# Kernel optimization log

Measured on AMD Instinct MI355X. Metric: run time of the kernel, lower is better.

The kernel has to match this reference:

```python
import jax, jax.numpy as jnp
import numpy as np

D, DK, DV, H = 1024, 64, 1024, 16
DVH = DV // H  # per-head value dim
EPS = 1e-5


def _layer_norm(x, g, b):
    mu = jnp.mean(x, axis=-1, keepdims=True)
    var = jnp.var(x, axis=-1, keepdims=True)
    return (x - mu) * jax.lax.rsqrt(var + EPS) * g + b


def setup_inputs() -> dict:
    key = jax.random.key(0)
    ks = jax.random.split(key, 12)
    s = lambda k, shape, fan_in: jax.random.normal(k, shape, jnp.float32) / np.sqrt(fan_in)
    return {
        "x": jax.random.normal(ks[0], (2, 2048, D), jnp.float32),
        "Wq": s(ks[1], (H, D, DK), D),
        "Wk": s(ks[2], (H, D, DK), D),
        "Wv": s(ks[3], (H, D, DVH), D),
        "Wo": s(ks[4], (DV, D), DV),
        "ln1_g": jnp.ones((D,), jnp.float32),
        "ln1_b": jnp.zeros((D,), jnp.float32),
        "W1": s(ks[5], (D, 4 * D), D),
        "b1": jnp.zeros((4 * D,), jnp.float32),
        "W2": s(ks[6], (4 * D, D), 4 * D),
        "b2": jnp.zeros((D,), jnp.float32),
        "ln2_g": jnp.ones((D,), jnp.float32),
        "ln2_b": jnp.zeros((D,), jnp.float32),
    }


def reference(x, Wq, Wk, Wv, Wo, ln1_g, ln1_b, W1, b1, W2, b2, ln2_g, ln2_b):
    B, S, _ = x.shape
    # per-head projections (vectorized over the head loop of the original)
    q = jnp.einsum("bsd,hdk->bhsk", x, Wq)
    k = jnp.einsum("bsd,hdk->bhsk", x, Wk)
    v = jnp.einsum("bsd,hdv->bhsv", x, Wv)
    scores = jnp.einsum("bhsk,bhtk->bhst", q, k) / np.sqrt(DK).astype(np.float32)
    attn = jax.nn.softmax(scores, axis=-1)
    o = jnp.einsum("bhst,bhtv->bhsv", attn, v)  # [B,H,S,DVH]
    o = o.transpose(0, 2, 1, 3).reshape(B, S, DV)  # concat heads
    attn_out = o @ Wo
    x1 = _layer_norm(attn_out + x, ln1_g, ln1_b)
    ffn = jax.nn.relu(x1 @ W1 + b1) @ W2 + b2
    return _layer_norm(ffn + x1, ln2_g, ln2_b)
```

## Files before the change

### kernel.cpp

```cpp
#include <hip/hip_runtime.h>
#include <hip/hip_bf16.h>

typedef unsigned short u16;
typedef unsigned int u32;
typedef short short8 __attribute__((ext_vector_type(8)));
typedef float fx4 __attribute__((ext_vector_type(4)));
typedef u32 ux4 __attribute__((ext_vector_type(4)));

__device__ __forceinline__ float b2f(u16 x) {
  return __uint_as_float(((u32)x) << 16);
}
__device__ __forceinline__ u16 f2b(float f) {
  u32 u = __float_as_uint(f);
  u += 0x7fffu + ((u >> 16) & 1u);
  return (u16)(u >> 16);
}
__device__ __forceinline__ u32 cvtpk(float a, float b) {
  u32 r;
  asm("v_cvt_pk_bf16_f32 %0, %1, %2" : "=v"(r) : "v"(a), "v"(b));
  return r;
}

__device__ __forceinline__ void load16(const u16* g, u16* l) {
  __builtin_amdgcn_global_load_lds(
      (__attribute__((address_space(1))) void*)(u16*)g,
      (__attribute__((address_space(3))) void*)l, 16, 0, 0);
}

__global__ __launch_bounds__(256) void cvt_f2b_kernel(
    const float* __restrict__ in, u16* __restrict__ out)
{
  int i = (blockIdx.x * 256 + threadIdx.x) * 4;
  fx4 v = *(const fx4*)(in + i);
  u16 o4[4];
#pragma unroll
  for (int j = 0; j < 4; ++j) o4[j] = f2b(v[j]);
  *(uint2*)(out + i) = *(uint2*)o4;
}

__global__ __launch_bounds__(256) void transpose_f2b_kernel(
    const float* __restrict__ in, u16* __restrict__ out,
    int R, int C, int out_ld)
{
  __shared__ __align__(16) u16 tile[32][33];
  int tx = threadIdx.x, ty = threadIdx.y;
  int c0 = blockIdx.x * 32, r0 = blockIdx.y * 32;
  const float* inb = in + (size_t)blockIdx.z * R * C;
  u16* outb = out + (size_t)blockIdx.z * C * out_ld;
#pragma unroll
  for (int i = 0; i < 4; ++i)
    tile[ty + i * 8][tx] = f2b(inb[(size_t)(r0 + ty + i * 8) * C + c0 + tx]);
  __syncthreads();
#pragma unroll
  for (int i = 0; i < 4; ++i)
    outb[(size_t)(c0 + ty + i * 8) * out_ld + r0 + tx] = tile[tx][ty + i * 8];
}

__global__ __launch_bounds__(256) void transpose_b2b_kernel(
    const u16* __restrict__ in, u16* __restrict__ out, int in_ld, int out_ld)
{
  __shared__ __align__(16) u16 tile[32][33];
  int tx = threadIdx.x, ty = threadIdx.y;
  int c0 = blockIdx.x * 32, r0 = blockIdx.y * 32;
#pragma unroll
  for (int i = 0; i < 4; ++i)
    tile[ty + i * 8][tx] = in[(size_t)(r0 + ty + i * 8) * in_ld + c0 + tx];
  __syncthreads();
#pragma unroll
  for (int i = 0; i < 4; ++i)
    out[(size_t)(c0 + ty + i * 8) * out_ld + r0 + tx] = tile[tx][ty + i * 8];
}

__global__ __launch_bounds__(256, 2) void gemm_bt(
    const u16* __restrict__ A, const u16* __restrict__ BT,
    const float* __restrict__ bias, void* __restrict__ Cp,
    int M, int N, int K, int flags)
{
  __shared__ __align__(16) u16 As[2][4096];
  __shared__ __align__(16) u16 Bs[2][4096];
  int tid = threadIdx.x;
  int lane = tid & 63, wid = tid >> 6;
  int l15 = lane & 15, quad = lane >> 4;
  int wm = wid >> 1, wn = wid & 1;
  int m0 = blockIdx.y * 128, n0 = blockIdx.x * 128;

  int srow = wid * 16 + (lane >> 2);
  int sswz = (((lane >> 2) & 3) + ((lane >> 4) & 3)) & 3;
  int gch = (lane & 3) ^ sswz;
  const u16* gA = A + (size_t)(m0 + srow) * K + gch * 8;
  const u16* gB = BT + (size_t)(n0 + srow) * K + gch * 8;
  size_t gstep = (size_t)64 * K;
  u16* lA = &As[0][wid * 512];
  u16* lB = &Bs[0][wid * 512];

  int rswz = ((l15 & 3) + (l15 >> 2)) & 3;
  int rphys = ((quad ^ rswz) & 3) << 3;

  fx4 acc[4][4];
#pragma unroll
  for (int i = 0; i < 4; ++i)
#pragma unroll
    for (int j = 0; j < 4; ++j) acc[i][j] = fx4{0.f, 0.f, 0.f, 0.f};

  int nt = K >> 5;
  load16(gA,         lA);
  load16(gA + gstep, lA + 2048);
  load16(gB,         lB);
  load16(gB + gstep, lB + 2048);

  for (int kt = 0; kt < nt; ++kt) {
    __syncthreads();
    if (kt + 1 < nt) {
      int buf = (kt + 1) & 1;
      const u16* ga = gA + (kt + 1) * 32;
      const u16* gb = gB + (kt + 1) * 32;
      load16(ga,         lA + buf * 4096);
      load16(ga + gstep, lA + buf * 4096 + 2048);
      load16(gb,         lB + buf * 4096);
      load16(gb + gstep, lB + buf * 4096 + 2048);
    }
    const u16* Ab = As[kt & 1];
    const u16* Bb = Bs[kt & 1];
    short8 af[4], bf[4];
#pragma unroll
    for (int t = 0; t < 4; ++t)
      af[t] = *(const short8*)&Ab[(wm * 64 + t * 16 + l15) * 32 + rphys];
#pragma unroll
    for (int t = 0; t < 4; ++t)
      bf[t] = *(const short8*)&Bb[(wn * 64 + t * 16 + l15) * 32 + rphys];
#pragma unroll
    for (int tm = 0; tm < 4; ++tm)
#pragma unroll
      for (int tn = 0; tn < 4; ++tn)
        acc[tm][tn] = __builtin_amdgcn_mfma_f32_16x16x32_bf16(
            af[tm], bf[tn], acc[tm][tn], 0, 0, 0);
  }

  bool obf = flags & 1, hb = flags & 2, rl = flags & 4;
#pragma unroll
  for (int tn = 0; tn < 4; ++tn) {
    int col = n0 + wn * 64 + tn * 16 + l15;
    float bv = hb ? bias[col] : 0.0f;
#pragma unroll
    for (int tm = 0; tm < 4; ++tm) {
      int row = m0 + wm * 64 + tm * 16 + (quad << 2);
#pragma unroll
      for (int r = 0; r < 4; ++r) {
        float v = acc[tm][tn][r] + bv;
        if (rl) v = fmaxf(v, 0.0f);
        size_t idx = (size_t)(row + r) * N + col;
        if (obf) ((u16*)Cp)[idx] = f2b(v);
        else ((float*)Cp)[idx] = v;
      }
    }
  }
}

__global__ __launch_bounds__(256, 2) void gemm_bt_n64(
    const u16* __restrict__ A, const u16* __restrict__ BT,
    const float* __restrict__ bias, void* __restrict__ Cp,
    int M, int N, int K, int flags)
{
  __shared__ __align__(16) u16 As[2][4096];
  __shared__ __align__(16) u16 Bs[2][2048];
  int tid = threadIdx.x;
  int lane = tid & 63, wid = tid >> 6;
  int l15 = lane & 15, quad = lane >> 4;
  int wm = wid >> 1, wn = wid & 1;
  int m0 = blockIdx.y * 128, n0 = blockIdx.x * 64;
  int zz = blockIdx.z;
  int kc = K / (int)gridDim.z;

  int srow = wid * 16 + (lane >> 2);
  int sswz = (((lane >> 2) & 3) + ((lane >> 4) & 3)) & 3;
  int gch = (lane & 3) ^ sswz;
  const u16* gA = A + (size_t)(m0 + srow) * K + zz * kc + gch * 8;
  const u16* gB = BT + (size_t)(n0 + srow) * K + zz * kc + gch * 8;
  size_t gstep = (size_t)64 * K;
  u16* lA = &As[0][wid * 512];
  u16* lB = &Bs[0][wid * 512];

  int rswz = ((l15 & 3) + (l15 >> 2)) & 3;
  int rphys = ((quad ^ rswz) & 3) << 3;

  fx4 acc[4][2];
#pragma unroll
  for (int i = 0; i < 4; ++i)
#pragma unroll
    for (int j = 0; j < 2; ++j) acc[i][j] = fx4{0.f, 0.f, 0.f, 0.f};

  int nt = kc >> 5;
  load16(gA,         lA);
  load16(gA + gstep, lA + 2048);
  load16(gB,         lB);

  for (int kt = 0; kt < nt; ++kt) {
    __syncthreads();
    if (kt + 1 < nt) {
      int buf = (kt + 1) & 1;
      const u16* ga = gA + (kt + 1) * 32;
      const u16* gb = gB + (kt + 1) * 32;
      load16(ga,         lA + buf * 4096);
      load16(ga + gstep, lA + buf * 4096 + 2048);
      load16(gb,         lB + buf * 2048);
    }
    const u16* Ab = As[kt & 1];
    const u16* Bb = Bs[kt & 1];
    short8 af[4], bf[2];
#pragma unroll
    for (int t = 0; t < 4; ++t)
      af[t] = *(const short8*)&Ab[(wm * 64 + t * 16 + l15) * 32 + rphys];
#pragma unroll
    for (int t = 0; t < 2; ++t)
      bf[t] = *(const short8*)&Bb[(wn * 32 + t * 16 + l15) * 32 + rphys];
#pragma unroll
    for (int tm = 0; tm < 4; ++tm)
#pragma unroll
      for (int tn = 0; tn < 2; ++tn)
        acc[tm][tn] = __builtin_amdgcn_mfma_f32_16x16x32_bf16(
            af[tm], bf[tn], acc[tm][tn], 0, 0, 0);
  }

  bool obf = flags & 1, hb = flags & 2, rl = flags & 4;
  u16* cb16 = (u16*)Cp + (size_t)zz * M * N;
  float* cf32 = (float*)Cp + (size_t)zz * M * N;
#pragma unroll
  for (int tn = 0; tn < 2; ++tn) {
    int col = n0 + wn * 32 + tn * 16 + l15;
    float bv = hb ? bias[col] : 0.0f;
#pragma unroll
    for (int tm = 0; tm < 4; ++tm) {
      int row = m0 + wm * 64 + tm * 16 + (quad << 2);
#pragma unroll
      for (int r = 0; r < 4; ++r) {
        float v = acc[tm][tn][r] + bv;
        if (rl) v = fmaxf(v, 0.0f);
        size_t idx = (size_t)(row + r) * N + col;
        if (obf) cb16[idx] = f2b(v);
        else cf32[idx] = v;
      }
    }
  }
}

__global__ __launch_bounds__(256) void attn_kernel(
    const u16* __restrict__ qkv, const u16* __restrict__ vT,
    u16* __restrict__ o)
{
  __shared__ __align__(16) u16 Ks[2][4096];
  __shared__ __align__(16) u16 Vs[2][4096];
  int tid = threadIdx.x;
  int lane = tid & 63, wid = tid >> 6;
  int l15 = lane & 15, quad = lane >> 4;
  int b = blockIdx.z, h = blockIdx.y;
  int q0 = blockIdx.x * 64 + wid * 16;

  const u16* qb = qkv + (size_t)(b * 2048 + q0 + l15) * 3072 + h * 64 + (quad << 3);
  short8 qf0 = *(const short8*)qb;
  short8 qf1 = *(const short8*)(qb + 32);

  int srow = tid >> 3;
  int gc8 = ((tid & 7) ^ (srow & 7)) << 3;
  const u16* kg = qkv + (size_t)(b * 2048 + srow) * 3072 + 1024 + h * 64 + gc8;
  const u16* vg = vT + (size_t)(h * 64 + srow) * 4096 + b * 2048 + gc8;
  u16* lk = &Ks[0][wid * 512];
  u16* lv = &Vs[0][wid * 512];

  fx4 oacc[4];
  float suml = 0.0f;
#pragma unroll
  for (int i = 0; i < 4; ++i) oacc[i] = fx4{0.f, 0.f, 0.f, 0.f};

  load16(kg,             lk);
  load16(kg + 32 * 3072, lk + 2048);
  load16(vg,             lv);
  load16(vg + 32 * 4096, lv + 2048);

  int swz = l15 & 7;
  int q2 = quad >> 1;
  int h4 = (quad & 1) * 4;
  for (int kt = 0; kt < 32; ++kt) {
    __syncthreads();
    if (kt + 1 < 32) {
      int buf = (kt + 1) & 1;
      const u16* kgn = kg + (size_t)(kt + 1) * 64 * 3072;
      const u16* vgn = vg + (kt + 1) * 64;
      load16(kgn,             lk + buf * 4096);
      load16(kgn + 32 * 3072, lk + buf * 4096 + 2048);
      load16(vgn,             lv + buf * 4096);
      load16(vgn + 32 * 4096, lv + buf * 4096 + 2048);
    }
    const u16* Kb = Ks[kt & 1];
    const u16* Vb = Vs[kt & 1];

    fx4 sc[4];
#pragma unroll
    for (int sub = 0; sub < 4; ++sub) {
      sc[sub] = fx4{0.f, 0.f, 0.f, 0.f};
      const u16* rp = &Kb[(sub * 16 + l15) * 64];
      short8 kf0 = *(const short8*)&rp[((quad ^ swz) & 7) << 3];
      short8 kf1 = *(const short8*)&rp[(((4 | quad) ^ swz) & 7) << 3];
      sc[sub] = __builtin_amdgcn_mfma_f32_16x16x32_bf16(kf0, qf0, sc[sub], 0, 0, 0);
      sc[sub] = __builtin_amdgcn_mfma_f32_16x16x32_bf16(kf1, qf1, sc[sub], 0, 0, 0);
    }

    u32 W[4][2];
    float ps = 0.0f;
#pragma unroll
    for (int sub = 0; sub < 4; ++sub) {
      float p0 = __expf(sc[sub][0] * 0.125f);
      float p1 = __expf(sc[sub][1] * 0.125f);
      float p2 = __expf(sc[sub][2] * 0.125f);
      float p3 = __expf(sc[sub][3] * 0.125f);
      ps += (p0 + p1) + (p2 + p3);
      W[sub][0] = cvtpk(p0, p1);
      W[sub][1] = cvtpk(p2, p3);
    }
    suml += ps;
    short8 pa1 = __builtin_bit_cast(short8, ux4{W[0][0], W[0][1], W[1][0], W[1][1]});
    short8 pa2 = __builtin_bit_cast(short8, ux4{W[2][0], W[2][1], W[3][0], W[3][1]});

#pragma unroll
    for (int dt = 0; dt < 4; ++dt) {
      const u16* rp = &Vb[(dt * 16 + l15) * 64];
      uint2 v0a = *(const uint2*)&rp[(((q2)     ^ swz) << 3) + h4];
      uint2 v0b = *(const uint2*)&rp[(((2 + q2) ^ swz) << 3) + h4];
      uint2 v1a = *(const uint2*)&rp[(((4 + q2) ^ swz) << 3) + h4];
      uint2 v1b = *(const uint2*)&rp[(((6 + q2) ^ swz) << 3) + h4];
      short8 vf0 = __builtin_bit_cast(short8, ux4{v0a.x, v0a.y, v0b.x, v0b.y});
      short8 vf1 = __builtin_bit_cast(short8, ux4{v1a.x, v1a.y, v1b.x, v1b.y});
      oacc[dt] = __builtin_amdgcn_mfma_f32_16x16x32_bf16(pa1, vf0, oacc[dt], 0, 0, 0);
      oacc[dt] = __builtin_amdgcn_mfma_f32_16x16x32_bf16(pa2, vf1, oacc[dt], 0, 0, 0);
    }
  }
  suml += __shfl_xor(suml, 16, 64);
  suml += __shfl_xor(suml, 32, 64);
  fx4 inv;
#pragma unroll
  for (int r = 0; r < 4; ++r)
    inv[r] = 1.0f / __shfl(suml, (quad << 2) + r, 64);
#pragma unroll
  for (int dt = 0; dt < 4; ++dt) {
    int col = h * 64 + dt * 16 + l15;
#pragma unroll
    for (int r = 0; r < 4; ++r)
      o[(size_t)(b * 2048 + q0 + (quad << 2) + r) * 1024 + col] =
          f2b(oacc[dt][r] * inv[r]);
  }
}

__global__ __launch_bounds__(256) void ln_kernel(
    const float* __restrict__ main0, const float* __restrict__ main1,
    const float* __restrict__ res, const float* __restrict__ cbias,
    const float* __restrict__ g, const float* __restrict__ beta,
    u16* __restrict__ out_b, float* __restrict__ out_f)
{
  __shared__ float red[8];
  int row = blockIdx.x, tid = threadIdx.x;
  size_t base = (size_t)row * 1024 + tid * 4;
  fx4 v = *(const fx4*)(main0 + base);
  fx4 v1 = *(const fx4*)(main1 + base);
  fx4 rv = *(const fx4*)(res + base);
#pragma unroll
  for (int i = 0; i < 4; ++i) v[i] += v1[i] + rv[i];
  if (cbias) {
    fx4 cb = *(const fx4*)(cbias + tid * 4);
#pragma unroll
    for (int i = 0; i < 4; ++i) v[i] += cb[i];
  }
  float s = v[0] + v[1] + v[2] + v[3];
  float sq = v[0] * v[0] + v[1] * v[1] + v[2] * v[2] + v[3] * v[3];
#pragma unroll
  for (int off = 32; off >= 1; off >>= 1) {
    s += __shfl_xor(s, off, 64);
    sq += __shfl_xor(sq, off, 64);
  }
  int wid = tid >> 6, lane = tid & 63;
  if (lane == 0) { red[wid] = s; red[wid + 4] = sq; }
  __syncthreads();
  float S = red[0] + red[1] + red[2] + red[3];
  float SQ = red[4] + red[5] + red[6] + red[7];
  float mean = S * (1.0f / 1024.0f);
  float var = SQ * (1.0f / 1024.0f) - mean * mean;
  float rs = rsqrtf(var + 1e-5f);
  fx4 gv = *(const fx4*)(g + tid * 4);
  fx4 bv = *(const fx4*)(beta + tid * 4);
  float of[4];
#pragma unroll
  for (int i = 0; i < 4; ++i) of[i] = (v[i] - mean) * rs * gv[i] + bv[i];
  if (out_f) *(fx4*)(out_f + base) = *(const fx4*)of;
  if (out_b) {
    u16 o4[4];
#pragma unroll
    for (int i = 0; i < 4; ++i) o4[i] = f2b(of[i]);
    *(uint2*)(out_b + base) = *(uint2*)o4;
  }
}

extern "C" void kernel_launch(void* const* d_in, const int* in_sizes, int n_in,
                              void* d_out, int out_size, void* d_ws, size_t ws_size,
                              hipStream_t stream) {
  (void)in_sizes; (void)n_in; (void)out_size; (void)ws_size;
  const float* x     = (const float*)d_in[0];
  const float* Wq    = (const float*)d_in[1];
  const float* Wk    = (const float*)d_in[2];
  const float* Wv    = (const float*)d_in[3];
  const float* Wo    = (const float*)d_in[4];
  const float* g1    = (const float*)d_in[5];
  const float* bb1   = (const float*)d_in[6];
  const float* W1    = (const float*)d_in[7];
  const float* bias1 = (const float*)d_in[8];
  const float* W2    = (const float*)d_in[9];
  const float* bias2 = (const float*)d_in[10];
  const float* g2    = (const float*)d_in[11];
  const float* bb2   = (const float*)d_in[12];

  char* ws = (char*)d_ws;
  const size_t MB = 1048576;
  u16* xb     = (u16*)(ws);
  u16* wqkvT  = (u16*)(ws + 8 * MB);
  u16* woT    = (u16*)(ws + 38 * MB);
  u16* qkv    = (u16*)(ws + 40 * MB);
  u16* vT     = (u16*)(ws + 64 * MB);
  u16* ob     = (u16*)(ws + 72 * MB);
  float* aout = (float*)(ws);
  u16* x1     = (u16*)(ws + 64 * MB);
  float* x1f  = (float*)(ws + 40 * MB);
  u16* w1T    = (u16*)(ws + 56 * MB);
  u16* w2T    = (u16*)(ws);
  u16* hbuf   = (u16*)(ws + 8 * MB);
  float* ffn  = (float*)(ws + 56 * MB);

  dim3 tb(32, 8, 1);
  cvt_f2b_kernel<<<4096, 256, 0, stream>>>(x, xb);
  transpose_f2b_kernel<<<dim3(2, 32, 16), tb, 0, stream>>>(Wq, wqkvT,           1024, 64, 1024);
  transpose_f2b_kernel<<<dim3(2, 32, 16), tb, 0, stream>>>(Wk, wqkvT + 1048576, 1024, 64, 1024);
  transpose_f2b_kernel<<<dim3(2, 32, 16), tb, 0, stream>>>(Wv, wqkvT + 2097152, 1024, 64, 1024);
  transpose_f2b_kernel<<<dim3(32, 32, 1), tb, 0, stream>>>(Wo, woT, 1024, 1024, 1024);

  gemm_bt<<<dim3(24, 32), 256, 0, stream>>>(xb, wqkvT, nullptr, qkv, 4096, 3072, 1024, 1);
  transpose_b2b_kernel<<<dim3(32, 128), tb, 0, stream>>>(qkv + 2048, vT, 3072, 4096);
  attn_kernel<<<dim3(32, 16, 2), 256, 0, stream>>>(qkv, vT, ob);
  gemm_bt_n64<<<dim3(16, 32, 2), 256, 0, stream>>>(ob, woT, nullptr, aout, 4096, 1024, 1024, 0);
  ln_kernel<<<4096, 256, 0, stream>>>(aout, aout + 4194304, x, nullptr, g1, bb1, x1, x1f);
  transpose_f2b_kernel<<<dim3(128, 32, 1), tb, 0, stream>>>(W1, w1T, 1024, 4096, 1024);
  transpose_f2b_kernel<<<dim3(32, 128, 1), tb, 0, stream>>>(W2, w2T, 4096, 1024, 4096);
  gemm_bt<<<dim3(32, 32), 256, 0, stream>>>(x1, w1T, bias1, hbuf, 4096, 4096, 1024, 1 | 2 | 4);
  gemm_bt_n64<<<dim3(16, 32, 2), 256, 0, stream>>>(hbuf, w2T, nullptr, ffn, 4096, 1024, 4096, 0);
  ln_kernel<<<4096, 256, 0, stream>>>(ffn, ffn + 4194304, x1f, bias2, g2, bb2, nullptr, (float*)d_out);
}
```

Before: 402.9 us.

## Permute K rows and use permlane32 swap for 128-bit V fragment reads in attention

The attention kernel remaps which K rows each lane loads, so the softmax probabilities can be rearranged into the P·V MFMA operand layout with permlane32_swap. V fragments then come from two 128-bit LDS reads instead of four 64-bit reads. It also replaces __expf with a raw exp2 and a prescaled constant, and raises wave priority around the MFMA blocks. The lane permutation is subtle and any mismatch between the row remap and the swap would silently corrupt results.

```diff
diff --git a/kernel.cpp b/kernel.cpp
--- a/kernel.cpp
+++ b/kernel.cpp
@@ -6,6 +6,7 @@
 typedef short short8 __attribute__((ext_vector_type(8)));
 typedef float fx4 __attribute__((ext_vector_type(4)));
 typedef u32 ux4 __attribute__((ext_vector_type(4)));
+typedef u32 ux2 __attribute__((ext_vector_type(2)));
 
 __device__ __forceinline__ float b2f(u16 x) {
   return __uint_as_float(((u32)x) << 16);
@@ -266,6 +267,11 @@
   u16* lk = &Ks[0][wid * 512];
   u16* lv = &Vs[0][wid * 512];
 
+  int lq = l15 >> 2;
+  int r0 = ((((lq & 1) << 1) | (lq >> 1)) << 2) | (l15 & 3);
+  int r1 = r0 ^ 4;
+  int sk0 = r0 & 7, sk1 = r1 & 7;
+
   fx4 oacc[4];
   float suml = 0.0f;
 #pragma unroll
@@ -277,8 +283,6 @@
   load16(vg + 32 * 4096, lv + 2048);
 
   int swz = l15 & 7;
-  int q2 = quad >> 1;
-  int h4 = (quad & 1) * 4;
   for (int kt = 0; kt < 32; ++kt) {
     __syncthreads();
     if (kt + 1 < 32) {
@@ -294,44 +298,56 @@
     const u16* Vb = Vs[kt & 1];
 
     fx4 sc[4];
+    __builtin_amdgcn_s_setprio(1);
 #pragma unroll
     for (int sub = 0; sub < 4; ++sub) {
+      int rs = (sub & 1) ? r1 : r0;
+      int sks = (sub & 1) ? sk1 : sk0;
       sc[sub] = fx4{0.f, 0.f, 0.f, 0.f};
-      const u16* rp = &Kb[(sub * 16 + l15) * 64];
-      short8 kf0 = *(const short8*)&rp[((quad ^ swz) & 7) << 3];
-      short8 kf1 = *(const short8*)&rp[(((4 | quad) ^ swz) & 7) << 3];
+      const u16* rp = &Kb[(sub * 16 + rs) * 64];
+      short8 kf0 = *(const short8*)&rp[((quad ^ sks) & 7) << 3];
+      short8 kf1 = *(const short8*)&rp[(((4 | quad) ^ sks) & 7) << 3];
       sc[sub] = __builtin_amdgcn_mfma_f32_16x16x32_bf16(kf0, qf0, sc[sub], 0, 0, 0);
       sc[sub] = __builtin_amdgcn_mfma_f32_16x16x32_bf16(kf1, qf1, sc[sub], 0, 0, 0);
     }
+    __builtin_amdgcn_s_setprio(0);
 
     u32 W[4][2];
     float ps = 0.0f;
 #pragma unroll
     for (int sub = 0; sub < 4; ++sub) {
-      float p0 = __expf(sc[sub][0] * 0.125f);
-      float p1 = __expf(sc[sub][1] * 0.125f);
-      float p2 = __expf(sc[sub][2] * 0.125f);
-      float p3 = __expf(sc[sub][3] * 0.125f);
+      float p0 = __builtin_amdgcn_exp2f(sc[sub][0] * 0.18033688011112042f);
+      float p1 = __builtin_amdgcn_exp2f(sc[sub][1] * 0.18033688011112042f);
+      float p2 = __builtin_amdgcn_exp2f(sc[sub][2] * 0.18033688011112042f);
+      float p3 = __builtin_amdgcn_exp2f(sc[sub][3] * 0.18033688011112042f);
       ps += (p0 + p1) + (p2 + p3);
       W[sub][0] = cvtpk(p0, p1);
       W[sub][1] = cvtpk(p2, p3);
     }
     suml += ps;
-    short8 pa1 = __builtin_bit_cast(short8, ux4{W[0][0], W[0][1], W[1][0], W[1][1]});
-    short8 pa2 = __builtin_bit_cast(short8, ux4{W[2][0], W[2][1], W[3][0], W[3][1]});
-
+
+    ux2 e00 = __builtin_amdgcn_permlane32_swap(W[0][0], W[1][0], false, false);
+    ux2 e01 = __builtin_amdgcn_permlane32_swap(W[0][1], W[1][1], false, false);
+    ux2 e10 = __builtin_amdgcn_permlane32_swap(W[2][0], W[3][0], false, false);
+    ux2 e11 = __builtin_amdgcn_permlane32_swap(W[2][1], W[3][1], false, false);
+    bool lo = lane < 32;
+    short8 pa1 = __builtin_bit_cast(short8,
+        ux4{lo ? e00[0] : e00[1], lo ? e01[0] : e01[1],
+            lo ? e00[1] : e00[0], lo ? e01[1] : e01[0]});
+    short8 pa2 = __builtin_bit_cast(short8,
+        ux4{lo ? e10[0] : e10[1], lo ? e11[0] : e11[1],
+            lo ? e10[1] : e10[0], lo ? e11[1] : e11[0]});
+
+    __builtin_amdgcn_s_setprio(1);
 #pragma unroll
     for (int dt = 0; dt < 4; ++dt) {
       const u16* rp = &Vb[(dt * 16 + l15) * 64];
-      uint2 v0a = *(const uint2*)&rp[(((q2)     ^ swz) << 3) + h4];
-      uint2 v0b = *(const uint2*)&rp[(((2 + q2) ^ swz) << 3) + h4];
-      uint2 v1a = *(const uint2*)&rp[(((4 + q2) ^ swz) << 3) + h4];
-      uint2 v1b = *(const uint2*)&rp[(((6 + q2) ^ swz) << 3) + h4];
-      short8 vf0 = __builtin_bit_cast(short8, ux4{v0a.x, v0a.y, v0b.x, v0b.y});
-      short8 vf1 = __builtin_bit_cast(short8, ux4{v1a.x, v1a.y, v1b.x, v1b.y});
+      short8 vf0 = *(const short8*)&rp[((quad ^ swz) & 7) << 3];
+      short8 vf1 = *(const short8*)&rp[(((4 | quad) ^ swz) & 7) << 3];
       oacc[dt] = __builtin_amdgcn_mfma_f32_16x16x32_bf16(pa1, vf0, oacc[dt], 0, 0, 0);
       oacc[dt] = __builtin_amdgcn_mfma_f32_16x16x32_bf16(pa2, vf1, oacc[dt], 0, 0, 0);
     }
+    __builtin_amdgcn_s_setprio(0);
   }
   suml += __shfl_xor(suml, 16, 64);
   suml += __shfl_xor(suml, 32, 64);
```

Measured after the change: 395.7 us. No clear change (-1.8%).
